# Optimization experiments

Hardware: AMD Instinct MI355X
Metric: run time of the kernel (lower is better)

Reference implementation:

```python
import jax, jax.numpy as jnp
import numpy as np

NEG_SLOPE = 0.2  # PyG GATConv default negative_slope
EPS = 1e-16     # PyG softmax denominator epsilon


def gat_conv(x, src, dst, W, a_src, a_dst, bias):
    """PyG GATConv (concat=True, dropout off). x:[N,Fin], src/dst:[E]."""
    N = x.shape[0]
    H, C = a_src.shape
    h = (x @ W).reshape(N, H, C)                      # per-head projected features
    es = jnp.einsum('nhc,hc->nh', h, a_src)           # alpha_src per node/head
    ed = jnp.einsum('nhc,hc->nh', h, a_dst)           # alpha_dst per node/head
    e = jax.nn.leaky_relu(es[src] + ed[dst], NEG_SLOPE)   # [E,H] edge scores
    # segment softmax over destination nodes (every node has a self loop)
    m = jax.ops.segment_max(e, dst, num_segments=N)
    p = jnp.exp(e - m[dst])
    denom = jax.ops.segment_sum(p, dst, num_segments=N)
    alpha = p / (denom[dst] + EPS)                    # [E,H]
    out = jax.ops.segment_sum(h[src] * alpha[:, :, None], dst, num_segments=N)
    return out.reshape(N, H * C) + bias


def _single_graph(x, ei, W1, a_src1, a_dst1, b1, W2, a_src2, a_dst2, b2):
    N = x.shape[0]
    loop = jnp.arange(N, dtype=ei.dtype)              # add_self_loops=True
    src = jnp.concatenate([ei[0], loop])
    dst = jnp.concatenate([ei[1], loop])
    h = jax.nn.relu(gat_conv(x, src, dst, W1, a_src1, a_dst1, b1))
    # F.dropout with p=0.0 is identity
    return gat_conv(h, src, dst, W2, a_src2, a_dst2, b2)


def setup_inputs() -> dict:
    key = jax.random.key(0)
    ks = jax.random.split(key, 9)
    B, N, E, F_in, H, C = 2, 20000, 320000, 128, 8, 64

    def glorot(k, shape):
        fan_in, fan_out = shape[-2] if len(shape) > 1 else shape[-1], shape[-1]
        s = np.sqrt(6.0 / (fan_in + fan_out)).astype(np.float32)
        return jax.random.uniform(k, shape, jnp.float32, -s, s)

    return {
        'xs': jax.random.normal(ks[0], (B, N, F_in), jnp.float32),
        'edge_indexs': jax.random.randint(ks[1], (B, 2, E), 0, N, jnp.int32),
        'W1': glorot(ks[2], (F_in, H * C)),
        'a_src1': glorot(ks[3], (H, C)),
        'a_dst1': glorot(ks[4], (H, C)),
        'b1': jnp.zeros((H * C,), jnp.float32),
        'W2': glorot(ks[5], (H * C, C)),
        'a_src2': glorot(ks[6], (1, C)),
        'a_dst2': glorot(ks[7], (1, C)),
        'b2': jnp.zeros((C,), jnp.float32),
    }


def reference(xs, edge_indexs, W1, a_src1, a_dst1, b1, W2, a_src2, a_dst2, b2):
    f = lambda x, ei: _single_graph(x, ei, W1, a_src1, a_dst1, b1, W2, a_src2, a_dst2, b2)
    return jax.vmap(f)(xs, edge_indexs)               # [B, N, C]
```

## Files before the change

### kernel.cpp

```cpp
#include <hip/hip_runtime.h>
#include <hip/hip_bf16.h>
#include <cstdint>

#define NEG_SLOPE 0.2f
#define SOFTMAX_EPS 1e-16f
#define NN 20000
#define EE 320000
#define CAP 48

typedef __hip_bfloat16 bf16;
typedef unsigned short ushort;
typedef short s8v __attribute__((ext_vector_type(8)));
typedef float f4v __attribute__((ext_vector_type(4)));

static __device__ __forceinline__ float lo16(unsigned u) { return __uint_as_float(u << 16); }
static __device__ __forceinline__ float hi16(unsigned u) { return __uint_as_float(u & 0xffff0000u); }
static __device__ __forceinline__ ushort f2bf(float v) {
    bf16 h = __float2bfloat16(v);
    return *(ushort*)&h;
}

__global__ void prep_kernel(const float* __restrict__ W1, const float* __restrict__ W2,
                            ushort* __restrict__ w1hi, ushort* __restrict__ w1lo,
                            ushort* __restrict__ w2hi, ushort* __restrict__ w2lo,
                            int* __restrict__ count) {
    int bid = blockIdx.x;
    int t = threadIdx.x;
    if (bid >= 48) {
        int idx = (bid - 48) * 256 + t;
        if (idx < 2 * NN) count[idx] = 0;
        return;
    }
    __shared__ float T[32][65];
    const float* src; ushort *dhi, *dlo; int K, C, c0, k0;
    if (bid < 32) { src = W1; dhi = w1hi; dlo = w1lo; K = 128; C = 512; c0 = (bid & 7) * 64; k0 = (bid >> 3) * 32; }
    else          { src = W2; dhi = w2hi; dlo = w2lo; K = 512; C = 64;  c0 = 0;              k0 = (bid - 32) * 32; }
    for (int i = 0; i < 8; ++i) {
        int flat = t + i * 256;
        int k = flat >> 6, c = flat & 63;
        T[k][c] = src[(size_t)(k0 + k) * C + c0 + c];
    }
    __syncthreads();
    int c = t >> 2, j0 = (t & 3) * 8;
    unsigned hp[4], lp[4];
#pragma unroll
    for (int p = 0; p < 4; ++p) {
        float v0 = T[j0 + p * 2][c], v1 = T[j0 + p * 2 + 1][c];
        ushort h0 = f2bf(v0), h1 = f2bf(v1);
        float l0 = v0 - __uint_as_float((unsigned)h0 << 16);
        float l1 = v1 - __uint_as_float((unsigned)h1 << 16);
        hp[p] = (unsigned)h0 | ((unsigned)h1 << 16);
        lp[p] = (unsigned)f2bf(l0) | ((unsigned)f2bf(l1) << 16);
    }
    size_t o = (size_t)(c0 + c) * K + k0 + j0;
    *(uint4*)&dhi[o] = make_uint4(hp[0], hp[1], hp[2], hp[3]);
    *(uint4*)&dlo[o] = make_uint4(lp[0], lp[1], lp[2], lp[3]);
}

#define G1S 40
#define GEMM1_BLOCKS 1252
__global__ __launch_bounds__(256) void gemm1_scatter(
        const float* __restrict__ xs, const ushort* __restrict__ w1hi,
        const ushort* __restrict__ w1lo, const float* __restrict__ a_src,
        const float* __restrict__ a_dst, bf16* __restrict__ h1,
        float* __restrict__ es, float* __restrict__ ed,
        const int* __restrict__ ei, int* __restrict__ count,
        ushort* __restrict__ esrc) {
    __shared__ ushort lds[25600];
    int t = threadIdx.x;
    int bid = blockIdx.x;

    if (bid >= GEMM1_BLOCKS) {
        int idx = bid - GEMM1_BLOCKS;
        int b = idx / 1250;
        int e = (idx % 1250) * 256 + t;
        const int* srcA = ei + (size_t)b * 2 * EE;
        int s = srcA[e], d = srcA[EE + e];
        if ((unsigned)d >= NN || (unsigned)s >= NN) return;
        int pos = atomicAdd(&count[b * NN + d], 1);
        if (pos < CAP)
            esrc[((size_t)b * NN + d) * CAP + pos] = (ushort)s;
        return;
    }

    ushort* Xhi = lds;
    ushort* Xlo = lds + 2560;
    ushort* Whi = lds + 5120;
    ushort* Wlo = lds + 15360;
    int w = t >> 6, lane = t & 63, quad = lane >> 4, l16 = lane & 15;
    int b = bid / 626;
    int rem = bid % 626;
    int nhalf = rem / 313;
    int row0 = (rem % 313) * 64, nbase = nhalf * 256;
    const float* x = xs + (size_t)b * NN * 128;
    bf16*  h1b = h1 + (size_t)b * NN * 512;
    float* esb = es + (size_t)b * NN * 8;
    float* edb = ed + (size_t)b * NN * 8;

    f4v acc[16];
#pragma unroll
    for (int i = 0; i < 16; ++i) acc[i] = (f4v)0.f;

    for (int kc = 0; kc < 4; ++kc) {
        __syncthreads();
        {
            int row = t >> 2, c0 = (t & 3) * 8;
            float v[8];
            if (row0 + row < NN) {
                float4 A = *(const float4*)&x[(size_t)(row0 + row) * 128 + kc * 32 + c0];
                float4 B = *(const float4*)&x[(size_t)(row0 + row) * 128 + kc * 32 + c0 + 4];
                v[0] = A.x; v[1] = A.y; v[2] = A.z; v[3] = A.w;
                v[4] = B.x; v[5] = B.y; v[6] = B.z; v[7] = B.w;
            } else {
#pragma unroll
                for (int i = 0; i < 8; ++i) v[i] = 0.f;
            }
            unsigned hp[4], lp[4];
#pragma unroll
            for (int p = 0; p < 4; ++p) {
                ushort h0 = f2bf(v[p * 2]), h1_ = f2bf(v[p * 2 + 1]);
                float l0 = v[p * 2] - __uint_as_float((unsigned)h0 << 16);
                float l1 = v[p * 2 + 1] - __uint_as_float((unsigned)h1_ << 16);
                hp[p] = (unsigned)h0 | ((unsigned)h1_ << 16);
                lp[p] = (unsigned)f2bf(l0) | ((unsigned)f2bf(l1) << 16);
            }
            *(uint4*)&Xhi[row * G1S + c0] = make_uint4(hp[0], hp[1], hp[2], hp[3]);
            *(uint4*)&Xlo[row * G1S + c0] = make_uint4(lp[0], lp[1], lp[2], lp[3]);
        }
        {
            const ushort* sh = w1hi + (size_t)(nbase + t) * 128 + kc * 32;
            const ushort* sl = w1lo + (size_t)(nbase + t) * 128 + kc * 32;
            uint4 h0 = *(const uint4*)(sh), h1_ = *(const uint4*)(sh + 8);
            uint4 h2 = *(const uint4*)(sh + 16), h3 = *(const uint4*)(sh + 24);
            uint4 l0 = *(const uint4*)(sl), l1 = *(const uint4*)(sl + 8);
            uint4 l2 = *(const uint4*)(sl + 16), l3 = *(const uint4*)(sl + 24);
            *(uint4*)&Whi[t * G1S]      = h0; *(uint4*)&Whi[t * G1S + 8]  = h1_;
            *(uint4*)&Whi[t * G1S + 16] = h2; *(uint4*)&Whi[t * G1S + 24] = h3;
            *(uint4*)&Wlo[t * G1S]      = l0; *(uint4*)&Wlo[t * G1S + 8]  = l1;
            *(uint4*)&Wlo[t * G1S + 16] = l2; *(uint4*)&Wlo[t * G1S + 24] = l3;
        }
        __syncthreads();
        int arow = (w * 16 + l16) * G1S + quad * 8;
        s8v ahi = *(const s8v*)&Xhi[arow];
        s8v alo = *(const s8v*)&Xlo[arow];
#pragma unroll
        for (int ct = 0; ct < 16; ++ct) {
            int baddr = (ct * 16 + l16) * G1S + quad * 8;
            s8v bhi = *(const s8v*)&Whi[baddr];
            s8v blo = *(const s8v*)&Wlo[baddr];
            acc[ct] = __builtin_amdgcn_mfma_f32_16x16x32_bf16(ahi, bhi, acc[ct], 0, 0, 0);
            acc[ct] = __builtin_amdgcn_mfma_f32_16x16x32_bf16(ahi, blo, acc[ct], 0, 0, 0);
            acc[ct] = __builtin_amdgcn_mfma_f32_16x16x32_bf16(alo, bhi, acc[ct], 0, 0, 0);
        }
    }

#pragma unroll
    for (int hh = 0; hh < 4; ++hh) {
        float s4[4] = {0.f, 0.f, 0.f, 0.f}, d4[4] = {0.f, 0.f, 0.f, 0.f};
#pragma unroll
        for (int ct4 = 0; ct4 < 4; ++ct4) {
            int ct = hh * 4 + ct4;
            int c = nbase + ct * 16 + l16;
            float as = a_src[c], ad = a_dst[c];
#pragma unroll
            for (int r = 0; r < 4; ++r) { s4[r] += acc[ct][r] * as; d4[r] += acc[ct][r] * ad; }
        }
#pragma unroll
        for (int o = 1; o < 16; o <<= 1) {
#pragma unroll
            for (int r = 0; r < 4; ++r) {
                s4[r] += __shfl_xor(s4[r], o);
                d4[r] += __shfl_xor(d4[r], o);
            }
        }
        if (l16 == 0) {
            int head = nhalf * 4 + hh;
#pragma unroll
            for (int r = 0; r < 4; ++r) {
                int gr = row0 + w * 16 + quad * 4 + r;
                if (gr < NN) { esb[gr * 8 + head] = s4[r]; edb[gr * 8 + head] = d4[r]; }
            }
        }
    }

    __syncthreads();
    ushort* rp = lds + w * 4224;
#pragma unroll
    for (int ct = 0; ct < 16; ++ct)
#pragma unroll
        for (int r = 0; r < 4; ++r)
            rp[(quad * 4 + r) * 264 + ct * 16 + l16] = f2bf(acc[ct][r]);
#pragma unroll
    for (int i = 0; i < 8; ++i) {
        int idx = i * 512 + lane * 8;
        int row = idx >> 8, col = idx & 255;
        uint4 vv = *(const uint4*)&rp[row * 264 + col];
        int gr = row0 + w * 16 + row;
        if (gr < NN) *(uint4*)&h1b[(size_t)gr * 512 + nbase + col] = vv;
    }
}

#define G2S 72
__global__ __launch_bounds__(256) void gemm2_mfma(
        const bf16* __restrict__ a, const ushort* __restrict__ w2hi,
        const ushort* __restrict__ w2lo, const float* __restrict__ a_src,
        const float* __restrict__ a_dst, bf16* __restrict__ h2,
        float* __restrict__ es, float* __restrict__ ed) {
    __shared__ ushort lds[13824];
    ushort* AS  = lds;
    ushort* Whi = lds + 4608;
    ushort* Wlo = lds + 9216;

    int t = threadIdx.x;
    int w = t >> 6, lane = t & 63, quad = lane >> 4, l16 = lane & 15;
    int b = blockIdx.y;
    int row0 = blockIdx.x * 64;
    const bf16* ab = a + (size_t)b * NN * 512;
    bf16*  h2b = h2 + (size_t)b * NN * 64;
    float* esb = es + (size_t)b * NN;
    float* edb = ed + (size_t)b * NN;

    f4v acc[4];
#pragma unroll
    for (int i = 0; i < 4; ++i) acc[i] = (f4v)0.f;

    for (int kc = 0; kc < 8; ++kc) {
        __syncthreads();
        {
            int row = t >> 2, k0 = (t & 3) * 16;
            uint4 q0, q1;
            if (row0 + row < NN) {
                q0 = *(const uint4*)(ab + (size_t)(row0 + row) * 512 + kc * 64 + k0);
                q1 = *(const uint4*)(ab + (size_t)(row0 + row) * 512 + kc * 64 + k0 + 8);
            } else { q0 = make_uint4(0, 0, 0, 0); q1 = q0; }
            *(uint4*)&AS[row * G2S + k0]     = q0;
            *(uint4*)&AS[row * G2S + k0 + 8] = q1;
            const ushort* sh = w2hi + (size_t)row * 512 + kc * 64 + k0;
            const ushort* sl = w2lo + (size_t)row * 512 + kc * 64 + k0;
            *(uint4*)&Whi[row * G2S + k0]     = *(const uint4*)(sh);
            *(uint4*)&Whi[row * G2S + k0 + 8] = *(const uint4*)(sh + 8);
            *(uint4*)&Wlo[row * G2S + k0]     = *(const uint4*)(sl);
            *(uint4*)&Wlo[row * G2S + k0 + 8] = *(const uint4*)(sl + 8);
        }
        __syncthreads();
#pragma unroll
        for (int ks = 0; ks < 2; ++ks) {
            s8v av = *(const s8v*)&AS[(w * 16 + l16) * G2S + ks * 32 + quad * 8];
#pragma unroll
            for (int ct = 0; ct < 4; ++ct) {
                int baddr = (ct * 16 + l16) * G2S + ks * 32 + quad * 8;
                s8v bhi = *(const s8v*)&Whi[baddr];
                s8v blo = *(const s8v*)&Wlo[baddr];
                acc[ct] = __builtin_amdgcn_mfma_f32_16x16x32_bf16(av, bhi, acc[ct], 0, 0, 0);
                acc[ct] = __builtin_amdgcn_mfma_f32_16x16x32_bf16(av, blo, acc[ct], 0, 0, 0);
            }
        }
    }

    {
        float s4[4] = {0.f, 0.f, 0.f, 0.f}, d4[4] = {0.f, 0.f, 0.f, 0.f};
#pragma unroll
        for (int ct = 0; ct < 4; ++ct) {
            int c = ct * 16 + l16;
            float as = a_src[c], ad = a_dst[c];
#pragma unroll
            for (int r = 0; r < 4; ++r) { s4[r] += acc[ct][r] * as; d4[r] += acc[ct][r] * ad; }
        }
#pragma unroll
        for (int o = 1; o < 16; o <<= 1) {
#pragma unroll
            for (int r = 0; r < 4; ++r) {
                s4[r] += __shfl_xor(s4[r], o);
                d4[r] += __shfl_xor(d4[r], o);
            }
        }
        if (l16 == 0) {
#pragma unroll
            for (int r = 0; r < 4; ++r) {
                int gr = row0 + w * 16 + quad * 4 + r;
                if (gr < NN) { esb[gr] = s4[r]; edb[gr] = d4[r]; }
            }
        }
    }

    __syncthreads();
    ushort* rp = lds + w * 1152;
#pragma unroll
    for (int ct = 0; ct < 4; ++ct)
#pragma unroll
        for (int r = 0; r < 4; ++r)
            rp[(quad * 4 + r) * G2S + ct * 16 + l16] = f2bf(acc[ct][r]);
#pragma unroll
    for (int i = 0; i < 2; ++i) {
        int idx = i * 512 + lane * 8;
        int row = idx >> 6, col = idx & 63;
        uint4 vv = *(const uint4*)&rp[row * G2S + col];
        int gr = row0 + w * 16 + row;
        if (gr < NN) *(uint4*)&h2b[(size_t)gr * 64 + col] = vv;
    }
}

__global__ __launch_bounds__(256) void aggregate1_kernel(
        const bf16* __restrict__ h1, const float* __restrict__ es,
        const float* __restrict__ ed, const int* __restrict__ count,
        const ushort* __restrict__ esrc, const float* __restrict__ b1,
        bf16* __restrict__ out1) {
    __shared__ float alds[4][8][68];
    int b = blockIdx.y;
    const bf16*  h1b = h1 + (size_t)b * NN * 512;
    const float* esb = es + (size_t)b * NN * 8;
    const float* edb = ed + (size_t)b * NN * 8;
    bf16* out1b = out1 + (size_t)b * NN * 512;

    int t = threadIdx.x;
    int wv = t >> 6, lane = t & 63;
    int n = blockIdx.x * 4 + wv;
    int deg_e = count[b * NN + n];
    deg_e = max(0, min(deg_e, CAP));
    int deg = deg_e + 1;
    size_t beg = ((size_t)b * NN + n) * CAP;

    float4 ed0 = *(const float4*)&edb[n * 8];
    float4 ed1 = *(const float4*)&edb[n * 8 + 4];
    float edh[8] = {ed0.x, ed0.y, ed0.z, ed0.w, ed1.x, ed1.y, ed1.z, ed1.w};

    int myhead = lane >> 3;
    float acc[8];
#pragma unroll
    for (int i = 0; i < 8; ++i) acc[i] = 0.f;

    bool act = lane < deg;
    int sreg = act ? ((lane < deg_e) ? (int)esrc[beg + lane] : n) : 0;
    float4 s0 = *(const float4*)&esb[(size_t)sreg * 8];
    float4 s1 = *(const float4*)&esb[(size_t)sreg * 8 + 4];
    float e[8] = {s0.x, s0.y, s0.z, s0.w, s1.x, s1.y, s1.z, s1.w};
    float m[8], p[8], sum[8];
#pragma unroll
    for (int h = 0; h < 8; ++h) {
        float v = e[h] + edh[h];
        v = (v >= 0.f) ? v : NEG_SLOPE * v;
        e[h] = act ? v : -1e30f;
        m[h] = e[h];
    }
#pragma unroll
    for (int o = 32; o > 0; o >>= 1) {
#pragma unroll
        for (int h = 0; h < 8; ++h) m[h] = fmaxf(m[h], __shfl_xor(m[h], o));
    }
#pragma unroll
    for (int h = 0; h < 8; ++h) { p[h] = act ? __expf(e[h] - m[h]) : 0.f; sum[h] = p[h]; }
#pragma unroll
    for (int o = 32; o > 0; o >>= 1) {
#pragma unroll
        for (int h = 0; h < 8; ++h) sum[h] += __shfl_xor(sum[h], o);
    }
#pragma unroll
    for (int h = 0; h < 8; ++h)
        alds[wv][h][lane] = p[h] / (sum[h] + SOFTMAX_EPS);

    int j = 0;
    for (; j + 3 < deg; j += 4) {
        int sa = __shfl(sreg, j),     sb = __shfl(sreg, j + 1);
        int sc = __shfl(sreg, j + 2), sd = __shfl(sreg, j + 3);
        float wa = alds[wv][myhead][j],     wb = alds[wv][myhead][j + 1];
        float wc = alds[wv][myhead][j + 2], wd = alds[wv][myhead][j + 3];
        uint4 ua = *(const uint4*)(h1b + (size_t)sa * 512 + lane * 8);
        uint4 ub = *(const uint4*)(h1b + (size_t)sb * 512 + lane * 8);
        uint4 uc = *(const uint4*)(h1b + (size_t)sc * 512 + lane * 8);
        uint4 ud = *(const uint4*)(h1b + (size_t)sd * 512 + lane * 8);
        acc[0] += wa * lo16(ua.x); acc[1] += wa * hi16(ua.x);
        acc[2] += wa * lo16(ua.y); acc[3] += wa * hi16(ua.y);
        acc[4] += wa * lo16(ua.z); acc[5] += wa * hi16(ua.z);
        acc[6] += wa * lo16(ua.w); acc[7] += wa * hi16(ua.w);
        acc[0] += wb * lo16(ub.x); acc[1] += wb * hi16(ub.x);
        acc[2] += wb * lo16(ub.y); acc[3] += wb * hi16(ub.y);
        acc[4] += wb * lo16(ub.z); acc[5] += wb * hi16(ub.z);
        acc[6] += wb * lo16(ub.w); acc[7] += wb * hi16(ub.w);
        acc[0] += wc * lo16(uc.x); acc[1] += wc * hi16(uc.x);
        acc[2] += wc * lo16(uc.y); acc[3] += wc * hi16(uc.y);
        acc[4] += wc * lo16(uc.z); acc[5] += wc * hi16(uc.z);
        acc[6] += wc * lo16(uc.w); acc[7] += wc * hi16(uc.w);
        acc[0] += wd * lo16(ud.x); acc[1] += wd * hi16(ud.x);
        acc[2] += wd * lo16(ud.y); acc[3] += wd * hi16(ud.y);
        acc[4] += wd * lo16(ud.z); acc[5] += wd * hi16(ud.z);
        acc[6] += wd * lo16(ud.w); acc[7] += wd * hi16(ud.w);
    }
    for (; j < deg; ++j) {
        int sa = __shfl(sreg, j);
        float wa = alds[wv][myhead][j];
        uint4 ua = *(const uint4*)(h1b + (size_t)sa * 512 + lane * 8);
        acc[0] += wa * lo16(ua.x); acc[1] += wa * hi16(ua.x);
        acc[2] += wa * lo16(ua.y); acc[3] += wa * hi16(ua.y);
        acc[4] += wa * lo16(ua.z); acc[5] += wa * hi16(ua.z);
        acc[6] += wa * lo16(ua.w); acc[7] += wa * hi16(ua.w);
    }

    float4 bv0 = *(const float4*)&b1[lane * 8];
    float4 bv1 = *(const float4*)&b1[lane * 8 + 4];
    float bias[8] = {bv0.x, bv0.y, bv0.z, bv0.w, bv1.x, bv1.y, bv1.z, bv1.w};
    union { ushort us[8]; uint4 u4; } pack;
#pragma unroll
    for (int i = 0; i < 8; ++i)
        pack.us[i] = f2bf(fmaxf(acc[i] + bias[i], 0.f));
    *(uint4*)(out1b + (size_t)n * 512 + lane * 8) = pack.u4;
}

__global__ void aggregate2_kernel(const bf16* __restrict__ h2, const float* __restrict__ es,
                                  const float* __restrict__ ed, const int* __restrict__ count,
                                  const ushort* __restrict__ esrc, const float* __restrict__ bias2,
                                  float* __restrict__ out) {
    __shared__ float wl[4][64];
    __shared__ int slidx[4][64];
    int b = blockIdx.y;
    const bf16*  h2b = h2 + (size_t)b * NN * 64;
    const float* esb = es + (size_t)b * NN;
    const float* edb = ed + (size_t)b * NN;
    float* outb = out + (size_t)b * NN * 64;

    int t = threadIdx.x;
    int wv = t >> 6, lane = t & 63;
    int n = blockIdx.x * 4 + wv;
    int deg_e = count[b * NN + n];
    deg_e = max(0, min(deg_e, CAP));
    int deg = deg_e + 1;
    size_t beg = ((size_t)b * NN + n) * CAP;
    float edn = edb[n];

    bool act = lane < deg;
    int sreg = act ? ((lane < deg_e) ? (int)esrc[beg + lane] : n) : 0;
    float ev = act ? esb[sreg] + edn : -1e30f;
    ev = (ev >= 0.f) ? ev : NEG_SLOPE * ev;
    if (!act) ev = -1e30f;
    float m = ev;
#pragma unroll
    for (int o = 32; o > 0; o >>= 1) m = fmaxf(m, __shfl_xor(m, o));
    float p = act ? __expf(ev - m) : 0.f;
    float sum = p;
#pragma unroll
    for (int o = 32; o > 0; o >>= 1) sum += __shfl_xor(sum, o);
    slidx[wv][lane] = sreg;
    wl[wv][lane] = p / (sum + SOFTMAX_EPS);

    float acc[4] = {0.f, 0.f, 0.f, 0.f};
    int grp = lane >> 4, ch4 = (lane & 15) * 4;
    int j = grp;
    for (; j + 4 < deg; j += 8) {
        int sA = slidx[wv][j];     float wA = wl[wv][j];
        int sB = slidx[wv][j + 4]; float wB = wl[wv][j + 4];
        uint2 uA = *(const uint2*)(h2b + (size_t)sA * 64 + ch4);
        uint2 uB = *(const uint2*)(h2b + (size_t)sB * 64 + ch4);
        acc[0] += wA * lo16(uA.x); acc[1] += wA * hi16(uA.x);
        acc[2] += wA * lo16(uA.y); acc[3] += wA * hi16(uA.y);
        acc[0] += wB * lo16(uB.x); acc[1] += wB * hi16(uB.x);
        acc[2] += wB * lo16(uB.y); acc[3] += wB * hi16(uB.y);
    }
    for (; j < deg; j += 4) {
        int s = slidx[wv][j];
        float wt = wl[wv][j];
        uint2 u = *(const uint2*)(h2b + (size_t)s * 64 + ch4);
        acc[0] += wt * lo16(u.x); acc[1] += wt * hi16(u.x);
        acc[2] += wt * lo16(u.y); acc[3] += wt * hi16(u.y);
    }
#pragma unroll
    for (int i = 0; i < 4; ++i) {
        acc[i] += __shfl_xor(acc[i], 16);
        acc[i] += __shfl_xor(acc[i], 32);
    }
    if (lane < 16) {
        float4 o4;
        o4.x = acc[0] + bias2[ch4 + 0];
        o4.y = acc[1] + bias2[ch4 + 1];
        o4.z = acc[2] + bias2[ch4 + 2];
        o4.w = acc[3] + bias2[ch4 + 3];
        *(float4*)&outb[(size_t)n * 64 + ch4] = o4;
    }
}

extern "C" void kernel_launch(void* const* d_in, const int* in_sizes, int n_in,
                              void* d_out, int out_size, void* d_ws, size_t ws_size,
                              hipStream_t stream) {
    const float* xs     = (const float*)d_in[0];
    const int*   ei     = (const int*)d_in[1];
    const float* W1     = (const float*)d_in[2];
    const float* a_src1 = (const float*)d_in[3];
    const float* a_dst1 = (const float*)d_in[4];
    const float* b1     = (const float*)d_in[5];
    const float* W2     = (const float*)d_in[6];
    const float* a_src2 = (const float*)d_in[7];
    const float* a_dst2 = (const float*)d_in[8];
    const float* b2     = (const float*)d_in[9];
    float* out = (float*)d_out;

    const int B = 2;

    uintptr_t p = (uintptr_t)d_ws;
    auto alloc = [&](size_t bytes) {
        void* r = (void*)p;
        p += (bytes + 255) & ~(size_t)255;
        return r;
    };
    bf16* h1   = (bf16*)alloc((size_t)B * NN * 512 * 2);
    bf16* out1 = (bf16*)alloc((size_t)B * NN * 512 * 2);
    char* unionA = (char*)alloc((size_t)B * NN * 64 * 2);
    float*  es1   = (float*)unionA;
    float*  ed1   = (float*)(unionA + 1280000);
    ushort* wt1hi = (ushort*)(unionA + 2560000);
    ushort* wt1lo = (ushort*)(unionA + 2560000 + 131072);
    bf16*   h2    = (bf16*)unionA;
    ushort* wt2hi = (ushort*)alloc((size_t)64 * 512 * 2);
    ushort* wt2lo = (ushort*)alloc((size_t)64 * 512 * 2);
    float* es2    = (float*)alloc((size_t)B * NN * 4);
    float* ed2    = (float*)alloc((size_t)B * NN * 4);
    int*   count  = (int*)alloc((size_t)B * NN * 4);
    ushort* esrc  = (ushort*)alloc((size_t)B * NN * CAP * 2);

    const int initBlocks = (2 * NN + 255) / 256;
    prep_kernel<<<48 + initBlocks, 256, 0, stream>>>(W1, W2, wt1hi, wt1lo, wt2hi, wt2lo, count);
    gemm1_scatter<<<GEMM1_BLOCKS + 2500, 256, 0, stream>>>(xs, wt1hi, wt1lo, a_src1, a_dst1,
                                                           h1, es1, ed1, ei, count, esrc);
    aggregate1_kernel<<<dim3(NN / 4, B), 256, 0, stream>>>(h1, es1, ed1, count, esrc, b1, out1);
    gemm2_mfma<<<dim3(313, B), 256, 0, stream>>>(out1, wt2hi, wt2lo, a_src2, a_dst2, h2, es2, ed2);
    aggregate2_kernel<<<dim3(NN / 4, B), 256, 0, stream>>>(h2, es2, ed2, count, esrc, b2, out);
}
```

Measured before the change: 271.5 us.

## Double-buffer neighbor row gathers in aggregate1 with packed FMA and LDS offsets

```diff
diff --git a/kernel.cpp b/kernel.cpp
--- a/kernel.cpp
+++ b/kernel.cpp
@@ -12,6 +12,7 @@
 typedef unsigned short ushort;
 typedef short s8v __attribute__((ext_vector_type(8)));
 typedef float f4v __attribute__((ext_vector_type(4)));
+typedef float f2v __attribute__((ext_vector_type(2)));
 
 static __device__ __forceinline__ float lo16(unsigned u) { return __uint_as_float(u << 16); }
 static __device__ __forceinline__ float hi16(unsigned u) { return __uint_as_float(u & 0xffff0000u); }
@@ -300,12 +301,13 @@
     }
 }
 
-__global__ __launch_bounds__(256) void aggregate1_kernel(
+__global__ __launch_bounds__(256, 8) void aggregate1_kernel(
         const bf16* __restrict__ h1, const float* __restrict__ es,
         const float* __restrict__ ed, const int* __restrict__ count,
         const ushort* __restrict__ esrc, const float* __restrict__ b1,
         bf16* __restrict__ out1) {
-    __shared__ float alds[4][8][68];
+    __shared__ float alds[4][8][60];
+    __shared__ unsigned offs[4][60];
     int b = blockIdx.y;
     const bf16*  h1b = h1 + (size_t)b * NN * 512;
     const float* esb = es + (size_t)b * NN * 8;
@@ -324,15 +326,12 @@
     float4 ed1 = *(const float4*)&edb[n * 8 + 4];
     float edh[8] = {ed0.x, ed0.y, ed0.z, ed0.w, ed1.x, ed1.y, ed1.z, ed1.w};
 
-    int myhead = lane >> 3;
-    float acc[8];
-#pragma unroll
-    for (int i = 0; i < 8; ++i) acc[i] = 0.f;
-
     bool act = lane < deg;
     int sreg = act ? ((lane < deg_e) ? (int)esrc[beg + lane] : n) : 0;
-    float4 s0 = *(const float4*)&esb[(size_t)sreg * 8];
-    float4 s1 = *(const float4*)&esb[(size_t)sreg * 8 + 4];
+    const char* eb = (const char*)esb;
+    unsigned eoff = (unsigned)sreg << 5;
+    float4 s0 = *(const float4*)(eb + eoff);
+    float4 s1 = *(const float4*)(eb + eoff + 16);
     float e[8] = {s0.x, s0.y, s0.z, s0.w, s1.x, s1.y, s1.z, s1.w};
     float m[8], p[8], sum[8];
 #pragma unroll
@@ -354,54 +353,66 @@
 #pragma unroll
         for (int h = 0; h < 8; ++h) sum[h] += __shfl_xor(sum[h], o);
     }
-#pragma unroll
-    for (int h = 0; h < 8; ++h)
-        alds[wv][h][lane] = p[h] / (sum[h] + SOFTMAX_EPS);
-
-    int j = 0;
-    for (; j + 3 < deg; j += 4) {
-        int sa = __shfl(sreg, j),     sb = __shfl(sreg, j + 1);
-        int sc = __shfl(sreg, j + 2), sd = __shfl(sreg, j + 3);
-        float wa = alds[wv][myhead][j],     wb = alds[wv][myhead][j + 1];
-        float wc = alds[wv][myhead][j + 2], wd = alds[wv][myhead][j + 3];
-        uint4 ua = *(const uint4*)(h1b + (size_t)sa * 512 + lane * 8);
-        uint4 ub = *(const uint4*)(h1b + (size_t)sb * 512 + lane * 8);
-        uint4 uc = *(const uint4*)(h1b + (size_t)sc * 512 + lane * 8);
-        uint4 ud = *(const uint4*)(h1b + (size_t)sd * 512 + lane * 8);
-        acc[0] += wa * lo16(ua.x); acc[1] += wa * hi16(ua.x);
-        acc[2] += wa * lo16(ua.y); acc[3] += wa * hi16(ua.y);
-        acc[4] += wa * lo16(ua.z); acc[5] += wa * hi16(ua.z);
-        acc[6] += wa * lo16(ua.w); acc[7] += wa * hi16(ua.w);
-        acc[0] += wb * lo16(ub.x); acc[1] += wb * hi16(ub.x);
-        acc[2] += wb * lo16(ub.y); acc[3] += wb * hi16(ub.y);
-        acc[4] += wb * lo16(ub.z); acc[5] += wb * hi16(ub.z);
-        acc[6] += wb * lo16(ub.w); acc[7] += wb * hi16(ub.w);
-        acc[0] += wc * lo16(uc.x); acc[1] += wc * hi16(uc.x);
-        acc[2] += wc * lo16(uc.y); acc[3] += wc * hi16(uc.y);
-        acc[4] += wc * lo16(uc.z); acc[5] += wc * hi16(uc.z);
-        acc[6] += wc * lo16(uc.w); acc[7] += wc * hi16(uc.w);
-        acc[0] += wd * lo16(ud.x); acc[1] += wd * hi16(ud.x);
-        acc[2] += wd * lo16(ud.y); acc[3] += wd * hi16(ud.y);
-        acc[4] += wd * lo16(ud.z); acc[5] += wd * hi16(ud.z);
-        acc[6] += wd * lo16(ud.w); acc[7] += wd * hi16(ud.w);
-    }
-    for (; j < deg; ++j) {
-        int sa = __shfl(sreg, j);
-        float wa = alds[wv][myhead][j];
-        uint4 ua = *(const uint4*)(h1b + (size_t)sa * 512 + lane * 8);
-        acc[0] += wa * lo16(ua.x); acc[1] += wa * hi16(ua.x);
-        acc[2] += wa * lo16(ua.y); acc[3] += wa * hi16(ua.y);
-        acc[4] += wa * lo16(ua.z); acc[5] += wa * hi16(ua.z);
-        acc[6] += wa * lo16(ua.w); acc[7] += wa * hi16(ua.w);
-    }
-
+    if (lane < 56) {
+        offs[wv][lane] = act ? ((unsigned)sreg << 10) : 0u;
+#pragma unroll
+        for (int h = 0; h < 8; ++h)
+            alds[wv][h][lane] = p[h] / (sum[h] + SOFTMAX_EPS);
+    }
+
+    int mh = lane >> 3;
+    unsigned l16b = (unsigned)lane * 16u;
+    const char* hb = (const char*)h1b;
+    int trips = (deg + 3) >> 2;
+
+    f2v acc0 = {0.f, 0.f}, acc1 = {0.f, 0.f}, acc2 = {0.f, 0.f}, acc3 = {0.f, 0.f};
+    uint4 A0, A1, A2, A3, B0, B1, B2, B3;
+    float4 wA, wB;
+
+#define LOADBANK(U0, U1, U2, U3, W4, blk) do { \
+        int s_ = (blk) << 2; \
+        uint4 ov_ = *(const uint4*)&offs[wv][s_]; \
+        W4 = *(const float4*)&alds[wv][mh][s_]; \
+        U0 = *(const uint4*)(hb + (ov_.x + l16b)); \
+        U1 = *(const uint4*)(hb + (ov_.y + l16b)); \
+        U2 = *(const uint4*)(hb + (ov_.z + l16b)); \
+        U3 = *(const uint4*)(hb + (ov_.w + l16b)); \
+    } while (0)
+
+#define ROW(U, W) do { \
+        f2v wp_ = {W, W}; \
+        f2v t0_ = {lo16(U.x), hi16(U.x)}; acc0 += t0_ * wp_; \
+        f2v t1_ = {lo16(U.y), hi16(U.y)}; acc1 += t1_ * wp_; \
+        f2v t2_ = {lo16(U.z), hi16(U.z)}; acc2 += t2_ * wp_; \
+        f2v t3_ = {lo16(U.w), hi16(U.w)}; acc3 += t3_ * wp_; \
+    } while (0)
+
+#define CONSUME(U0, U1, U2, U3, W4) do { \
+        ROW(U0, W4.x); ROW(U1, W4.y); ROW(U2, W4.z); ROW(U3, W4.w); \
+    } while (0)
+
+    LOADBANK(A0, A1, A2, A3, wA, 0);
+    LOADBANK(B0, B1, B2, B3, wB, 1);
+    int it = 0;
+    for (; it + 2 < trips; it += 2) {
+        CONSUME(A0, A1, A2, A3, wA); LOADBANK(A0, A1, A2, A3, wA, it + 2);
+        CONSUME(B0, B1, B2, B3, wB); LOADBANK(B0, B1, B2, B3, wB, it + 3);
+    }
+    CONSUME(A0, A1, A2, A3, wA);
+    if (it + 1 < trips) CONSUME(B0, B1, B2, B3, wB);
+
+#undef LOADBANK
+#undef ROW
+#undef CONSUME
+
+    float accs[8] = {acc0.x, acc0.y, acc1.x, acc1.y, acc2.x, acc2.y, acc3.x, acc3.y};
     float4 bv0 = *(const float4*)&b1[lane * 8];
     float4 bv1 = *(const float4*)&b1[lane * 8 + 4];
     float bias[8] = {bv0.x, bv0.y, bv0.z, bv0.w, bv1.x, bv1.y, bv1.z, bv1.w};
     union { ushort us[8]; uint4 u4; } pack;
 #pragma unroll
     for (int i = 0; i < 8; ++i)
-        pack.us[i] = f2bf(fmaxf(acc[i] + bias[i], 0.f));
+        pack.us[i] = f2bf(fmaxf(accs[i] + bias[i], 0.f));
     *(uint4*)(out1b + (size_t)n * 512 + lane * 8) = pack.u4;
 }
 
```

After: 294.0 us. 1.08x slower.
